# Kernel tuning notes

Hardware: AMD Instinct MI355X
Metric: run time of the kernel (lower is better)

## Reference

```python
import math
import jax, jax.numpy as jnp
import numpy as np

D_MODEL = 1024
N_HEADS = 16


def setup_inputs() -> dict:
    key = jax.random.key(0)
    ks = jax.random.split(key, 5)
    B, S, D = 4, 2048, D_MODEL
    std = math.sqrt(2.0 / (D + D))
    x = jax.random.normal(ks[0], (B, S, D), dtype=jnp.float32)
    wq = jax.random.normal(ks[1], (D, D), dtype=jnp.float32) * std
    wk = jax.random.normal(ks[2], (D, D), dtype=jnp.float32) * std
    wv = jax.random.normal(ks[3], (D, D), dtype=jnp.float32) * std
    wo = jax.random.normal(ks[4], (D, D), dtype=jnp.float32) * std
    return {"x": x, "wq": wq, "wk": wk, "wv": wv, "wo": wo}


def reference(x, wq, wk, wv, wo):
    B, S, D = x.shape
    H = N_HEADS
    dk = D // H
    # projections: weight is (d_out, d_in) -> y_...j = x_...i W_ji
    def proj(w):
        y = jnp.einsum('bsi,ji->bsj', x, w)
        return y.reshape(B, S, H, dk).transpose(0, 2, 1, 3)  # b h s dk
    Q, K, V = proj(wq), proj(wk), proj(wv)
    scores = jnp.einsum('bhnd,bhmd->bhnm', Q, K) / math.sqrt(dk)
    causal = jnp.tril(jnp.ones((S, S), dtype=bool))  # True = attend
    scores = jnp.where(causal, scores, -jnp.inf)
    weights = jax.nn.softmax(scores, axis=-1)
    attn = jnp.einsum('bhnm,bhmd->bhnd', weights, V)
    attn = attn.transpose(0, 2, 1, 3).reshape(B, S, D)
    return jnp.einsum('bsi,ji->bsj', attn, wo)
```

## Files before the change

### kernel.cpp

```cpp
#include <hip/hip_runtime.h>
#include <hip/hip_bf16.h>
#include <cstdint>

#define D_MODEL 1024
#define NHEADS  16
#define DK      64
#define BATCH   4
#define SEQ     2048
#define MROWS   (BATCH * SEQ)
#define NQT2    (SEQ / 128)
#define NW_ELEM (D_MODEL * D_MODEL)

#define QSCALE 0.18033688011112042f

typedef __attribute__((ext_vector_type(4))) float  f32x4;
typedef __attribute__((ext_vector_type(8))) __bf16 bf16x8;
typedef __attribute__((ext_vector_type(8))) short  short8;

__device__ __forceinline__ unsigned short f2bf(float f) {
    unsigned int u = __float_as_uint(f);
    unsigned int r = (u + 0x7fffu + ((u >> 16) & 1u)) >> 16;
    return (unsigned short)r;
}

__device__ __forceinline__ unsigned int cvtpk_bf16(float lo, float hi) {
    unsigned int r;
    asm volatile("v_cvt_pk_bf16_f32 %0, %1, %2" : "=v"(r) : "v"(lo), "v"(hi));
    return r;
}

__device__ __forceinline__ float exp2_raw(float x) {
    float r;
    asm("v_exp_f32 %0, %1" : "=v"(r) : "v"(x));
    return r;
}

__device__ __forceinline__ void permlane32_swap(unsigned int& a, unsigned int& b) {
    asm("v_permlane32_swap_b32 %0, %1" : "+v"(a), "+v"(b));
}
__device__ __forceinline__ void permlane16_swap(unsigned int& a, unsigned int& b) {
    asm("v_permlane16_swap_b32 %0, %1" : "+v"(a), "+v"(b));
}

__global__ void cvt_bf16(const float* __restrict__ in, unsigned short* __restrict__ out, int n) {
    int i = (blockIdx.x * 256 + threadIdx.x) * 4;
    if (i >= n) return;
    float4 v = *reinterpret_cast<const float4*>(in + i);
    ushort4 o;
    o.x = f2bf(v.x); o.y = f2bf(v.y); o.z = f2bf(v.z); o.w = f2bf(v.w);
    *reinterpret_cast<ushort4*>(out + i) = o;
}

__global__ void cvt_bf16_w(const float* __restrict__ w0, const float* __restrict__ w1,
                           const float* __restrict__ w2, const float* __restrict__ w3,
                           unsigned short* __restrict__ o0, unsigned short* __restrict__ o1,
                           unsigned short* __restrict__ o2, unsigned short* __restrict__ o3,
                           int n) {
    const int z = blockIdx.y;
    const float* in = (z == 0) ? w0 : (z == 1) ? w1 : (z == 2) ? w2 : w3;
    unsigned short* out = (z == 0) ? o0 : (z == 1) ? o1 : (z == 2) ? o2 : o3;
    int i = (blockIdx.x * 256 + threadIdx.x) * 4;
    if (i >= n) return;
    float4 v = *reinterpret_cast<const float4*>(in + i);
    ushort4 o;
    o.x = f2bf(v.x); o.y = f2bf(v.y); o.z = f2bf(v.z); o.w = f2bf(v.w);
    *reinterpret_cast<ushort4*>(out + i) = o;
}

__device__ __forceinline__ void gload_lds16(const void* g, void* l) {
    __builtin_amdgcn_global_load_lds(
        (const __attribute__((address_space(1))) void*)(uintptr_t)g,
        (__attribute__((address_space(3))) void*)(unsigned int)(uintptr_t)l,
        16, 0, 0);
}

#define BM 128
#define BN 128
#define BK 32

__global__ __launch_bounds__(256, 2) void gemm_qkv(
    const unsigned short* __restrict__ A,
    const unsigned short* __restrict__ W,
    unsigned short* __restrict__ Cq,
    unsigned short* __restrict__ Ck,
    unsigned short* __restrict__ Cv)
{
    __shared__ __align__(16) unsigned short As[2][BM * BK];
    __shared__ __align__(16) unsigned short Bs[3][2][BN * BK];

    const int K = D_MODEL, N = D_MODEL;
    const int tid  = threadIdx.x;
    const int wave = tid >> 6;
    const int lane = tid & 63;
    const int wr   = wave >> 1;
    const int wc   = wave & 1;
    const int bm   = blockIdx.x * BM;
    const int bn   = blockIdx.y * BN;

    f32x4 acc[3][4][4];
    #pragma unroll
    for (int w = 0; w < 3; w++)
        #pragma unroll
        for (int i = 0; i < 4; i++)
            #pragma unroll
            for (int j = 0; j < 4; j++)
                #pragma unroll
                for (int r = 0; r < 4; r++) acc[w][i][j][r] = 0.f;

    const int srow = tid >> 2;
    const int scol = (tid & 3) * 8;

    const int kg = (lane >> 4) * 8;
    const int rl = lane & 15;

    const unsigned short* Arow0 = A + (size_t)(bm + srow) * K + scol;
    const unsigned short* Arow1 = A + (size_t)(bm + 64 + srow) * K + scol;
    const unsigned short* Wrow0 = W + (size_t)(bn + srow) * K + scol;
    const unsigned short* Wrow1 = W + (size_t)(bn + 64 + srow) * K + scol;

    auto STAGE = [&](int buf, int k0) {
        gload_lds16(Arow0 + k0, &As[buf][0] + wave * 512);
        gload_lds16(Arow1 + k0, &As[buf][0] + 2048 + wave * 512);
        #pragma unroll
        for (int w = 0; w < 3; w++) {
            gload_lds16(Wrow0 + (size_t)w * NW_ELEM + k0, &Bs[w][buf][0] + wave * 512);
            gload_lds16(Wrow1 + (size_t)w * NW_ELEM + k0, &Bs[w][buf][0] + 2048 + wave * 512);
        }
    };

    auto COMPUTE = [&](int buf) {
        bf16x8 a[4];
        #pragma unroll
        for (int mi = 0; mi < 4; mi++) {
            short8 t = *reinterpret_cast<const short8*>(&As[buf][(wr * 64 + mi * 16 + rl) * BK + kg]);
            a[mi] = __builtin_bit_cast(bf16x8, t);
        }
        #pragma unroll
        for (int w = 0; w < 3; w++)
            #pragma unroll
            for (int ni = 0; ni < 4; ni++) {
                short8 t = *reinterpret_cast<const short8*>(&Bs[w][buf][(wc * 64 + ni * 16 + rl) * BK + kg]);
                bf16x8 b = __builtin_bit_cast(bf16x8, t);
                #pragma unroll
                for (int mi = 0; mi < 4; mi++)
                    acc[w][mi][ni] = __builtin_amdgcn_mfma_f32_16x16x32_bf16(a[mi], b, acc[w][mi][ni], 0, 0, 0);
            }
    };

    const int NT = K / BK;

    STAGE(0, 0);
    __syncthreads();

    int cur = 0;
    for (int t = 0; t < NT - 1; ++t) {
        STAGE(cur ^ 1, (t + 1) * BK);
        COMPUTE(cur);
        __syncthreads();
        cur ^= 1;
    }
    COMPUTE(cur);

    const int rg = (lane >> 4) * 4;
    #pragma unroll
    for (int w = 0; w < 3; w++) {
        unsigned short* C = (w == 0) ? Cq : (w == 1) ? Ck : Cv;
        const float cs = (w == 0) ? QSCALE : 1.0f;
        #pragma unroll
        for (int mi = 0; mi < 4; mi++)
            #pragma unroll
            for (int ni = 0; ni < 4; ni++)
                #pragma unroll
                for (int r = 0; r < 4; r++) {
                    int row = bm + wr * 64 + mi * 16 + rg + r;
                    int col = bn + wc * 64 + ni * 16 + rl;
                    C[(size_t)row * N + col] = f2bf(acc[w][mi][ni][r] * cs);
                }
    }
}

__global__ __launch_bounds__(256) void gemm_out(
    const unsigned short* __restrict__ A,
    const unsigned short* __restrict__ Bt,
    float* __restrict__ C)
{
    __shared__ __align__(16) unsigned short As[2][BM * BK];
    __shared__ __align__(16) unsigned short Bs[2][BN * BK];

    const int K = D_MODEL, N = D_MODEL;
    const int tid  = threadIdx.x;
    const int wave = tid >> 6;
    const int lane = tid & 63;
    const int wr   = wave >> 1;
    const int wc   = wave & 1;
    const int bm   = blockIdx.x * BM;
    const int bn   = blockIdx.y * BN;

    f32x4 acc[4][4];
    #pragma unroll
    for (int i = 0; i < 4; i++)
        #pragma unroll
        for (int j = 0; j < 4; j++)
            #pragma unroll
            for (int r = 0; r < 4; r++) acc[i][j][r] = 0.f;

    const int srow = tid >> 2;
    const int scol = (tid & 3) * 8;

    const int kg = (lane >> 4) * 8;
    const int rl = lane & 15;

    const unsigned short* Arow0 = A  + (size_t)(bm + srow) * K + scol;
    const unsigned short* Arow1 = A  + (size_t)(bm + 64 + srow) * K + scol;
    const unsigned short* Brow0 = Bt + (size_t)(bn + srow) * K + scol;
    const unsigned short* Brow1 = Bt + (size_t)(bn + 64 + srow) * K + scol;

    auto STAGE = [&](int buf, int k0) {
        gload_lds16(Arow0 + k0, &As[buf][0] + wave * 512);
        gload_lds16(Arow1 + k0, &As[buf][0] + 2048 + wave * 512);
        gload_lds16(Brow0 + k0, &Bs[buf][0] + wave * 512);
        gload_lds16(Brow1 + k0, &Bs[buf][0] + 2048 + wave * 512);
    };

    auto COMPUTE = [&](int buf) {
        bf16x8 a[4], b[4];
        #pragma unroll
        for (int mi = 0; mi < 4; mi++) {
            short8 t = *reinterpret_cast<const short8*>(&As[buf][(wr * 64 + mi * 16 + rl) * BK + kg]);
            a[mi] = __builtin_bit_cast(bf16x8, t);
        }
        #pragma unroll
        for (int ni = 0; ni < 4; ni++) {
            short8 t = *reinterpret_cast<const short8*>(&Bs[buf][(wc * 64 + ni * 16 + rl) * BK + kg]);
            b[ni] = __builtin_bit_cast(bf16x8, t);
        }
        #pragma unroll
        for (int mi = 0; mi < 4; mi++)
            #pragma unroll
            for (int ni = 0; ni < 4; ni++)
                acc[mi][ni] = __builtin_amdgcn_mfma_f32_16x16x32_bf16(a[mi], b[ni], acc[mi][ni], 0, 0, 0);
    };

    const int NT = K / BK;

    STAGE(0, 0);
    __syncthreads();

    int cur = 0;
    for (int t = 0; t < NT - 1; ++t) {
        STAGE(cur ^ 1, (t + 1) * BK);
        COMPUTE(cur);
        __syncthreads();
        cur ^= 1;
    }
    COMPUTE(cur);

    const int rg = (lane >> 4) * 4;
    #pragma unroll
    for (int mi = 0; mi < 4; mi++)
        #pragma unroll
        for (int ni = 0; ni < 4; ni++)
            #pragma unroll
            for (int r = 0; r < 4; r++) {
                int row = bm + wr * 64 + mi * 16 + rg + r;
                int col = bn + wc * 64 + ni * 16 + rl;
                C[(size_t)row * N + col] = acc[mi][ni][r];
            }
}

__global__ __launch_bounds__(512, 4) void attn_mfma(
    const unsigned short* __restrict__ Q,
    const unsigned short* __restrict__ K,
    const unsigned short* __restrict__ V,
    unsigned short* __restrict__ O)
{
    __shared__ __align__(16) unsigned short Ks[2][64 * 64];
    __shared__ __align__(16) unsigned short Vt[2][64 * 64];

    const int bh  = blockIdx.x;
    const int b   = bh >> 4;
    const int h   = bh & 15;
    const int qt  = NQT2 - 1 - blockIdx.y;
    const int tid = threadIdx.x;
    const int wave = tid >> 6;
    const int lane = tid & 63;
    const int lg   = lane >> 4;
    const int lq   = lane & 15;

    const size_t base = ((size_t)b * SEQ) * D_MODEL + h * DK;
    const unsigned short* Kb = K + base;
    const unsigned short* Vb = V + base;

    const int qw  = qt * 128 + wave * 16;
    const int myq = qw + lq;

    bf16x8 qf[2];
    {
        const unsigned short* qp = Q + base + (size_t)myq * D_MODEL + lg * 8;
        qf[0] = __builtin_bit_cast(bf16x8, *reinterpret_cast<const short8*>(qp));
        qf[1] = __builtin_bit_cast(bf16x8, *reinterpret_cast<const short8*>(qp + 32));
    }

    const short8 ones_s = {(short)0x3F80, (short)0x3F80, (short)0x3F80, (short)0x3F80,
                           (short)0x3F80, (short)0x3F80, (short)0x3F80, (short)0x3F80};
    const bf16x8 onesf = __builtin_bit_cast(bf16x8, ones_s);

    f32x4 acc[4];
    f32x4 acc_l;
    #pragma unroll
    for (int i = 0; i < 4; i++)
        #pragma unroll
        for (int r = 0; r < 4; r++) acc[i][r] = 0.f;
    #pragma unroll
    for (int r = 0; r < 4; r++) acc_l[r] = 0.f;
    float m_run = -INFINITY;

    const int trow  = tid >> 3;
    const int tslot = tid & 7;
    const unsigned short* Ksrc = Kb + (size_t)trow * D_MODEL + (tslot ^ (trow & 7)) * 8;

    const unsigned short* Vsrc = Vb + (size_t)lane * D_MODEL + wave * 8;
    union { uint4 v; unsigned short u[8]; } vpre;

    const int nt = 2 * qt + 2;

    gload_lds16(Ksrc, &Ks[0][0] + wave * 512);
    vpre.v = *reinterpret_cast<const uint4*>(Vsrc);
    #pragma unroll
    for (int e = 0; e < 8; ++e) {
        const int addr = (wave * 8 + e) * 128 + ((lane * 2) ^ (e << 4));
        *reinterpret_cast<unsigned short*>((char*)&Vt[0][0] + addr) = vpre.u[e];
    }
    __syncthreads();

    for (int t = 0; t < nt; ++t) {
        const int c = t & 1;
        const bool pf = (t + 1 < nt);

        if (pf) {
            const size_t moff = (size_t)(t + 1) * 64 * D_MODEL;
            gload_lds16(Ksrc + moff, &Ks[c ^ 1][0] + wave * 512);
            vpre.v = *reinterpret_cast<const uint4*>(Vsrc + moff);
        }

        const int m0 = t * 64;

        if (m0 <= qw + 15) {
            f32x4 s[4];
            __builtin_amdgcn_s_setprio(1);
            #pragma unroll
            for (int kg = 0; kg < 4; ++kg) {
                #pragma unroll
                for (int r = 0; r < 4; ++r) s[kg][r] = 0.f;
                #pragma unroll
                for (int ks = 0; ks < 2; ++ks) {
                    const int row  = kg * 16 + lq;
                    const int slot = (ks * 4 + lg) ^ (row & 7);
                    bf16x8 kf = __builtin_bit_cast(bf16x8,
                        *reinterpret_cast<const short8*>((const char*)&Ks[c][0] + row * 128 + slot * 16));
                    s[kg] = __builtin_amdgcn_mfma_f32_16x16x32_bf16(kf, qf[ks], s[kg], 0, 0, 0);
                }
            }
            __builtin_amdgcn_s_setprio(0);

            if (m0 + 63 > qw) {
                #pragma unroll
                for (int kg = 0; kg < 4; ++kg)
                    #pragma unroll
                    for (int r = 0; r < 4; ++r)
                        if (m0 + kg * 16 + lg * 4 + r > myq) s[kg][r] = -INFINITY;
            }
            const float a0 = fmaxf(fmaxf(s[0][0], s[0][1]), fmaxf(s[0][2], s[0][3]));
            const float a1 = fmaxf(fmaxf(s[1][0], s[1][1]), fmaxf(s[1][2], s[1][3]));
            const float a2 = fmaxf(fmaxf(s[2][0], s[2][1]), fmaxf(s[2][2], s[2][3]));
            const float a3 = fmaxf(fmaxf(s[3][0], s[3][1]), fmaxf(s[3][2], s[3][3]));
            float mx = fmaxf(fmaxf(a0, a1), fmaxf(a2, a3));
            mx = fmaxf(mx, __shfl_xor(mx, 16));
            mx = fmaxf(mx, __shfl_xor(mx, 32));

            if (!__all(mx <= m_run + 12.f)) {
                const float mnew = fmaxf(m_run, mx);
                const float sc   = exp2_raw(m_run - mnew);
                m_run = mnew;
                float scv[4];
                #pragma unroll
                for (int r = 0; r < 4; ++r) scv[r] = __shfl(sc, lg * 4 + r);
                #pragma unroll
                for (int dg = 0; dg < 4; ++dg)
                    #pragma unroll
                    for (int r = 0; r < 4; ++r) acc[dg][r] *= scv[r];
                #pragma unroll
                for (int r = 0; r < 4; ++r) acc_l[r] *= scv[r];
            }

            float p[4][4];
            #pragma unroll
            for (int kg = 0; kg < 4; ++kg)
                #pragma unroll
                for (int r = 0; r < 4; ++r)
                    p[kg][r] = exp2_raw(s[kg][r] - m_run);

            #pragma unroll
            for (int ks = 0; ks < 2; ++ks) {
                unsigned int A0 = cvtpk_bf16(p[2*ks][0],   p[2*ks][1]);
                unsigned int A1 = cvtpk_bf16(p[2*ks][2],   p[2*ks][3]);
                unsigned int B0 = cvtpk_bf16(p[2*ks+1][0], p[2*ks+1][1]);
                unsigned int B1 = cvtpk_bf16(p[2*ks+1][2], p[2*ks+1][3]);
                permlane32_swap(A0, B0);
                permlane16_swap(A0, B0);
                permlane32_swap(A1, B1);
                permlane16_swap(A1, B1);
                uint4 awv = make_uint4(A0, A1, B0, B1);
                bf16x8 af = __builtin_bit_cast(bf16x8, awv);
                __builtin_amdgcn_s_setprio(1);
                #pragma unroll
                for (int dg = 0; dg < 4; ++dg) {
                    const int d = dg * 16 + lq;
                    const int addr = d * 128 + ((ks * 64 + lg * 16) ^ ((d & 7) << 4));
                    bf16x8 vf = __builtin_bit_cast(bf16x8,
                        *reinterpret_cast<const short8*>((const char*)&Vt[c][0] + addr));
                    acc[dg] = __builtin_amdgcn_mfma_f32_16x16x32_bf16(af, vf, acc[dg], 0, 0, 0);
                }
                acc_l = __builtin_amdgcn_mfma_f32_16x16x32_bf16(af, onesf, acc_l, 0, 0, 0);
                __builtin_amdgcn_s_setprio(0);
            }
        }

        if (pf) {
            #pragma unroll
            for (int e = 0; e < 8; ++e) {
                const int addr = (wave * 8 + e) * 128 + ((lane * 2) ^ (e << 4));
                *reinterpret_cast<unsigned short*>((char*)&Vt[c ^ 1][0] + addr) = vpre.u[e];
            }
        }
        __syncthreads();
    }

    float lv[4];
    #pragma unroll
    for (int r = 0; r < 4; ++r) lv[r] = 1.0f / acc_l[r];
    #pragma unroll
    for (int dg = 0; dg < 4; ++dg)
        #pragma unroll
        for (int r = 0; r < 4; ++r) {
            const int qrow = qw + lg * 4 + r;
            O[base + (size_t)qrow * D_MODEL + dg * 16 + lq] = f2bf(acc[dg][r] * lv[r]);
        }
}

extern "C" void kernel_launch(void* const* d_in, const int* in_sizes, int n_in,
                              void* d_out, int out_size, void* d_ws, size_t ws_size,
                              hipStream_t stream) {
    const float* x  = (const float*)d_in[0];
    const float* wq = (const float*)d_in[1];
    const float* wk = (const float*)d_in[2];
    const float* wv = (const float*)d_in[3];
    const float* wo = (const float*)d_in[4];

    char* ws = (char*)d_ws;
    const size_t NXB = (size_t)MROWS * D_MODEL * 2;
    const size_t NWB = (size_t)D_MODEL * D_MODEL * 2;

    unsigned short* xb  = (unsigned short*)(ws);
    unsigned short* wqb = (unsigned short*)(ws + NXB);
    unsigned short* wkb = (unsigned short*)(ws + NXB + NWB);
    unsigned short* wvb = (unsigned short*)(ws + NXB + 2 * NWB);
    unsigned short* wob = (unsigned short*)(ws + NXB + 3 * NWB);
    unsigned short* Qb  = (unsigned short*)(ws + NXB + 4 * NWB);
    unsigned short* Kb  = (unsigned short*)(ws + NXB + 4 * NWB + NXB);
    unsigned short* Vb  = (unsigned short*)(ws + NXB + 4 * NWB + 2 * NXB);
    unsigned short* Ab  = (unsigned short*)(ws + NXB + 4 * NWB + 3 * NXB);

    const int NX = MROWS * D_MODEL;
    const int NW = D_MODEL * D_MODEL;

    cvt_bf16<<<NX / 1024, 256, 0, stream>>>(x, xb, NX);
    dim3 gw(NW / 1024, 4, 1);
    cvt_bf16_w<<<gw, 256, 0, stream>>>(wq, wk, wv, wo, wqb, wkb, wvb, wob, NW);

    dim3 gqkv(MROWS / BM, D_MODEL / BN, 1);
    gemm_qkv<<<gqkv, 256, 0, stream>>>(xb, wqb, Qb, Kb, Vb);

    dim3 gattn(BATCH * NHEADS, NQT2, 1);
    attn_mfma<<<gattn, 512, 0, stream>>>(Qb, Kb, Vb, Ab);

    dim3 gout(MROWS / BM, D_MODEL / BN, 1);
    gemm_out<<<gout, 256, 0, stream>>>(Ab, wob, (float*)d_out);
}
```

Measured before the change: 164.2 us.

## Process two 16-row query groups per wave to double K/V tile reuse

Each wave now handles 32 query rows (two 16-row groups) instead of 16, so every attention block covers 256 queries and each K/V tile loaded into LDS feeds twice as many MFMAs. The grid shrinks to 8 query tiles per head, and block ordering is changed to interleave heavy and light causal tiles. This is meant to cut global/LDS K/V traffic and barrier overhead per unit of work. In exchange it raises register pressure under launch_bounds(512,4), halves the number of blocks, and adds more wasted work on diagonal tiles.

```diff
diff --git a/kernel.cpp b/kernel.cpp
--- a/kernel.cpp
+++ b/kernel.cpp
@@ -8,7 +8,7 @@
 #define BATCH   4
 #define SEQ     2048
 #define MROWS   (BATCH * SEQ)
-#define NQT2    (SEQ / 128)
+#define NQT3    (SEQ / 256)
 #define NW_ELEM (D_MODEL * D_MODEL)
 
 #define QSCALE 0.18033688011112042f
@@ -280,7 +280,8 @@
     const int bh  = blockIdx.x;
     const int b   = bh >> 4;
     const int h   = bh & 15;
-    const int qt  = NQT2 - 1 - blockIdx.y;
+    const int y   = blockIdx.y;
+    const int qt  = (y < 4) ? (7 - y) : (y - 4);
     const int tid = threadIdx.x;
     const int wave = tid >> 6;
     const int lane = tid & 63;
@@ -291,29 +292,35 @@
     const unsigned short* Kb = K + base;
     const unsigned short* Vb = V + base;
 
-    const int qw  = qt * 128 + wave * 16;
+    const int qw  = qt * 256 + wave * 32;
     const int myq = qw + lq;
 
-    bf16x8 qf[2];
+    bf16x8 qf[2][2];
     {
-        const unsigned short* qp = Q + base + (size_t)myq * D_MODEL + lg * 8;
-        qf[0] = __builtin_bit_cast(bf16x8, *reinterpret_cast<const short8*>(qp));
-        qf[1] = __builtin_bit_cast(bf16x8, *reinterpret_cast<const short8*>(qp + 32));
+        const unsigned short* qp0 = Q + base + (size_t)myq * D_MODEL + lg * 8;
+        qf[0][0] = __builtin_bit_cast(bf16x8, *reinterpret_cast<const short8*>(qp0));
+        qf[0][1] = __builtin_bit_cast(bf16x8, *reinterpret_cast<const short8*>(qp0 + 32));
+        const unsigned short* qp1 = qp0 + 16 * D_MODEL;
+        qf[1][0] = __builtin_bit_cast(bf16x8, *reinterpret_cast<const short8*>(qp1));
+        qf[1][1] = __builtin_bit_cast(bf16x8, *reinterpret_cast<const short8*>(qp1 + 32));
     }
 
     const short8 ones_s = {(short)0x3F80, (short)0x3F80, (short)0x3F80, (short)0x3F80,
                            (short)0x3F80, (short)0x3F80, (short)0x3F80, (short)0x3F80};
     const bf16x8 onesf = __builtin_bit_cast(bf16x8, ones_s);
 
-    f32x4 acc[4];
-    f32x4 acc_l;
-    #pragma unroll
-    for (int i = 0; i < 4; i++)
-        #pragma unroll
-        for (int r = 0; r < 4; r++) acc[i][r] = 0.f;
-    #pragma unroll
-    for (int r = 0; r < 4; r++) acc_l[r] = 0.f;
-    float m_run = -INFINITY;
+    f32x4 acc[2][4];
+    f32x4 acc_l[2];
+    #pragma unroll
+    for (int g = 0; g < 2; g++) {
+        #pragma unroll
+        for (int i = 0; i < 4; i++)
+            #pragma unroll
+            for (int r = 0; r < 4; r++) acc[g][i][r] = 0.f;
+        #pragma unroll
+        for (int r = 0; r < 4; r++) acc_l[g][r] = 0.f;
+    }
+    float m_run0 = -INFINITY, m_run1 = -INFINITY;
 
     const int trow  = tid >> 3;
     const int tslot = tid & 7;
@@ -322,7 +329,7 @@
     const unsigned short* Vsrc = Vb + (size_t)lane * D_MODEL + wave * 8;
     union { uint4 v; unsigned short u[8]; } vpre;
 
-    const int nt = 2 * qt + 2;
+    const int nt = 4 * qt + 4;
 
     gload_lds16(Ksrc, &Ks[0][0] + wave * 512);
     vpre.v = *reinterpret_cast<const uint4*>(Vsrc);
@@ -345,20 +352,21 @@
 
         const int m0 = t * 64;
 
-        if (m0 <= qw + 15) {
-            f32x4 s[4];
+        if (m0 <= qw + 31) {
+            f32x4 s0[4], s1[4];
             __builtin_amdgcn_s_setprio(1);
             #pragma unroll
             for (int kg = 0; kg < 4; ++kg) {
                 #pragma unroll
-                for (int r = 0; r < 4; ++r) s[kg][r] = 0.f;
+                for (int r = 0; r < 4; ++r) { s0[kg][r] = 0.f; s1[kg][r] = 0.f; }
                 #pragma unroll
                 for (int ks = 0; ks < 2; ++ks) {
                     const int row  = kg * 16 + lq;
                     const int slot = (ks * 4 + lg) ^ (row & 7);
                     bf16x8 kf = __builtin_bit_cast(bf16x8,
                         *reinterpret_cast<const short8*>((const char*)&Ks[c][0] + row * 128 + slot * 16));
-                    s[kg] = __builtin_amdgcn_mfma_f32_16x16x32_bf16(kf, qf[ks], s[kg], 0, 0, 0);
+                    s0[kg] = __builtin_amdgcn_mfma_f32_16x16x32_bf16(kf, qf[0][ks], s0[kg], 0, 0, 0);
+                    s1[kg] = __builtin_amdgcn_mfma_f32_16x16x32_bf16(kf, qf[1][ks], s1[kg], 0, 0, 0);
                 }
             }
             __builtin_amdgcn_s_setprio(0);
@@ -367,51 +375,87 @@
                 #pragma unroll
                 for (int kg = 0; kg < 4; ++kg)
                     #pragma unroll
-                    for (int r = 0; r < 4; ++r)
-                        if (m0 + kg * 16 + lg * 4 + r > myq) s[kg][r] = -INFINITY;
-            }
-            const float a0 = fmaxf(fmaxf(s[0][0], s[0][1]), fmaxf(s[0][2], s[0][3]));
-            const float a1 = fmaxf(fmaxf(s[1][0], s[1][1]), fmaxf(s[1][2], s[1][3]));
-            const float a2 = fmaxf(fmaxf(s[2][0], s[2][1]), fmaxf(s[2][2], s[2][3]));
-            const float a3 = fmaxf(fmaxf(s[3][0], s[3][1]), fmaxf(s[3][2], s[3][3]));
-            float mx = fmaxf(fmaxf(a0, a1), fmaxf(a2, a3));
-            mx = fmaxf(mx, __shfl_xor(mx, 16));
-            mx = fmaxf(mx, __shfl_xor(mx, 32));
-
-            if (!__all(mx <= m_run + 12.f)) {
-                const float mnew = fmaxf(m_run, mx);
-                const float sc   = exp2_raw(m_run - mnew);
-                m_run = mnew;
+                    for (int r = 0; r < 4; ++r) {
+                        const int key = m0 + kg * 16 + lg * 4 + r;
+                        if (key > myq)      s0[kg][r] = -INFINITY;
+                        if (key > myq + 16) s1[kg][r] = -INFINITY;
+                    }
+            }
+
+            const float a00 = fmaxf(fmaxf(s0[0][0], s0[0][1]), fmaxf(s0[0][2], s0[0][3]));
+            const float a01 = fmaxf(fmaxf(s0[1][0], s0[1][1]), fmaxf(s0[1][2], s0[1][3]));
+            const float a02 = fmaxf(fmaxf(s0[2][0], s0[2][1]), fmaxf(s0[2][2], s0[2][3]));
+            const float a03 = fmaxf(fmaxf(s0[3][0], s0[3][1]), fmaxf(s0[3][2], s0[3][3]));
+            float mx0 = fmaxf(fmaxf(a00, a01), fmaxf(a02, a03));
+            mx0 = fmaxf(mx0, __shfl_xor(mx0, 16));
+            mx0 = fmaxf(mx0, __shfl_xor(mx0, 32));
+            const float a10 = fmaxf(fmaxf(s1[0][0], s1[0][1]), fmaxf(s1[0][2], s1[0][3]));
+            const float a11 = fmaxf(fmaxf(s1[1][0], s1[1][1]), fmaxf(s1[1][2], s1[1][3]));
+            const float a12 = fmaxf(fmaxf(s1[2][0], s1[2][1]), fmaxf(s1[2][2], s1[2][3]));
+            const float a13 = fmaxf(fmaxf(s1[3][0], s1[3][1]), fmaxf(s1[3][2], s1[3][3]));
+            float mx1 = fmaxf(fmaxf(a10, a11), fmaxf(a12, a13));
+            mx1 = fmaxf(mx1, __shfl_xor(mx1, 16));
+            mx1 = fmaxf(mx1, __shfl_xor(mx1, 32));
+
+            if (!__all(mx0 <= m_run0 + 12.f)) {
+                const float mnew = fmaxf(m_run0, mx0);
+                const float sc   = exp2_raw(m_run0 - mnew);
+                m_run0 = mnew;
                 float scv[4];
                 #pragma unroll
                 for (int r = 0; r < 4; ++r) scv[r] = __shfl(sc, lg * 4 + r);
                 #pragma unroll
                 for (int dg = 0; dg < 4; ++dg)
                     #pragma unroll
-                    for (int r = 0; r < 4; ++r) acc[dg][r] *= scv[r];
-                #pragma unroll
-                for (int r = 0; r < 4; ++r) acc_l[r] *= scv[r];
-            }
-
-            float p[4][4];
+                    for (int r = 0; r < 4; ++r) acc[0][dg][r] *= scv[r];
+                #pragma unroll
+                for (int r = 0; r < 4; ++r) acc_l[0][r] *= scv[r];
+            }
+            if (!__all(mx1 <= m_run1 + 12.f)) {
+                const float mnew = fmaxf(m_run1, mx1);
+                const float sc   = exp2_raw(m_run1 - mnew);
+                m_run1 = mnew;
+                float scv[4];
+                #pragma unroll
+                for (int r = 0; r < 4; ++r) scv[r] = __shfl(sc, lg * 4 + r);
+                #pragma unroll
+                for (int dg = 0; dg < 4; ++dg)
+                    #pragma unroll
+                    for (int r = 0; r < 4; ++r) acc[1][dg][r] *= scv[r];
+                #pragma unroll
+                for (int r = 0; r < 4; ++r) acc_l[1][r] *= scv[r];
+            }
+
             #pragma unroll
             for (int kg = 0; kg < 4; ++kg)
                 #pragma unroll
-                for (int r = 0; r < 4; ++r)
-                    p[kg][r] = exp2_raw(s[kg][r] - m_run);
+                for (int r = 0; r < 4; ++r) {
+                    s0[kg][r] = exp2_raw(s0[kg][r] - m_run0);
+                    s1[kg][r] = exp2_raw(s1[kg][r] - m_run1);
+                }
 
             #pragma unroll
             for (int ks = 0; ks < 2; ++ks) {
-                unsigned int A0 = cvtpk_bf16(p[2*ks][0],   p[2*ks][1]);
-                unsigned int A1 = cvtpk_bf16(p[2*ks][2],   p[2*ks][3]);
-                unsigned int B0 = cvtpk_bf16(p[2*ks+1][0], p[2*ks+1][1]);
-                unsigned int B1 = cvtpk_bf16(p[2*ks+1][2], p[2*ks+1][3]);
+                unsigned int A0 = cvtpk_bf16(s0[2*ks][0],   s0[2*ks][1]);
+                unsigned int A1 = cvtpk_bf16(s0[2*ks][2],   s0[2*ks][3]);
+                unsigned int B0 = cvtpk_bf16(s0[2*ks+1][0], s0[2*ks+1][1]);
+                unsigned int B1 = cvtpk_bf16(s0[2*ks+1][2], s0[2*ks+1][3]);
                 permlane32_swap(A0, B0);
                 permlane16_swap(A0, B0);
                 permlane32_swap(A1, B1);
                 permlane16_swap(A1, B1);
-                uint4 awv = make_uint4(A0, A1, B0, B1);
-                bf16x8 af = __builtin_bit_cast(bf16x8, awv);
+                bf16x8 af0 = __builtin_bit_cast(bf16x8, make_uint4(A0, A1, B0, B1));
+
+                unsigned int C0 = cvtpk_bf16(s1[2*ks][0],   s1[2*ks][1]);
+                unsigned int C1 = cvtpk_bf16(s1[2*ks][2],   s1[2*ks][3]);
+                unsigned int D0 = cvtpk_bf16(s1[2*ks+1][0], s1[2*ks+1][1]);
+                unsigned int D1 = cvtpk_bf16(s1[2*ks+1][2], s1[2*ks+1][3]);
+                permlane32_swap(C0, D0);
+                permlane16_swap(C0, D0);
+                permlane32_swap(C1, D1);
+                permlane16_swap(C1, D1);
+                bf16x8 af1 = __builtin_bit_cast(bf16x8, make_uint4(C0, C1, D0, D1));
+
                 __builtin_amdgcn_s_setprio(1);
                 #pragma unroll
                 for (int dg = 0; dg < 4; ++dg) {
@@ -419,9 +463,11 @@
                     const int addr = d * 128 + ((ks * 64 + lg * 16) ^ ((d & 7) << 4));
                     bf16x8 vf = __builtin_bit_cast(bf16x8,
                         *reinterpret_cast<const short8*>((const char*)&Vt[c][0] + addr));
-                    acc[dg] = __builtin_amdgcn_mfma_f32_16x16x32_bf16(af, vf, acc[dg], 0, 0, 0);
+                    acc[0][dg] = __builtin_amdgcn_mfma_f32_16x16x32_bf16(af0, vf, acc[0][dg], 0, 0, 0);
+                    acc[1][dg] = __builtin_amdgcn_mfma_f32_16x16x32_bf16(af1, vf, acc[1][dg], 0, 0, 0);
                 }
-                acc_l = __builtin_amdgcn_mfma_f32_16x16x32_bf16(af, onesf, acc_l, 0, 0, 0);
+                acc_l[0] = __builtin_amdgcn_mfma_f32_16x16x32_bf16(af0, onesf, acc_l[0], 0, 0, 0);
+                acc_l[1] = __builtin_amdgcn_mfma_f32_16x16x32_bf16(af1, onesf, acc_l[1], 0, 0, 0);
                 __builtin_amdgcn_s_setprio(0);
             }
         }
@@ -436,16 +482,19 @@
         __syncthreads();
     }
 
-    float lv[4];
-    #pragma unroll
-    for (int r = 0; r < 4; ++r) lv[r] = 1.0f / acc_l[r];
-    #pragma unroll
-    for (int dg = 0; dg < 4; ++dg)
-        #pragma unroll
-        for (int r = 0; r < 4; ++r) {
-            const int qrow = qw + lg * 4 + r;
-            O[base + (size_t)qrow * D_MODEL + dg * 16 + lq] = f2bf(acc[dg][r] * lv[r]);
-        }
+    #pragma unroll
+    for (int g = 0; g < 2; ++g) {
+        float lv[4];
+        #pragma unroll
+        for (int r = 0; r < 4; ++r) lv[r] = 1.0f / acc_l[g][r];
+        #pragma unroll
+        for (int dg = 0; dg < 4; ++dg)
+            #pragma unroll
+            for (int r = 0; r < 4; ++r) {
+                const int qrow = qw + g * 16 + lg * 4 + r;
+                O[base + (size_t)qrow * D_MODEL + dg * 16 + lq] = f2bf(acc[g][dg][r] * lv[r]);
+            }
+    }
 }
 
 extern "C" void kernel_launch(void* const* d_in, const int* in_sizes, int n_in,
@@ -481,7 +530,7 @@
     dim3 gqkv(MROWS / BM, D_MODEL / BN, 1);
     gemm_qkv<<<gqkv, 256, 0, stream>>>(xb, wqb, Qb, Kb, Vb);
 
-    dim3 gattn(BATCH * NHEADS, NQT2, 1);
+    dim3 gattn(BATCH * NHEADS, NQT3, 1);
     attn_mfma<<<gattn, 512, 0, stream>>>(Qb, Kb, Vb, Ab);
 
     dim3 gout(MROWS / BM, D_MODEL / BN, 1);
```

New measurement: 172.3 us. 1.05x slower.
